# Optimization experiments

Hardware: AMD Instinct MI355X
Metric: run time of the kernel (lower is better)

The kernel has to match this reference:

```python
import jax, jax.numpy as jnp
import numpy as np

NUM_SAMPLES = 100


def setup_inputs() -> dict:
    key = jax.random.key(0)
    # [B, 2C, H, W]: first C channels are logits, last C are log-std
    inp = jax.random.normal(key, (8, 38, 256, 256), dtype=jnp.float32)
    return {"input": inp}


def reference(input):
    logits, log_std = jnp.split(input, 2, axis=-3)  # each [B, C, H, W]
    std = jnp.exp(log_std)
    keys = jax.random.split(jax.random.key(1), NUM_SAMPLES)

    def body(acc, k):
        eps = jax.random.normal(k, std.shape, dtype=std.dtype)
        acc = acc + jax.nn.softmax(logits + eps * std, axis=-3)
        return acc, None

    softmax_sum, _ = jax.lax.scan(body, jnp.zeros_like(logits), keys)
    return softmax_sum / NUM_SAMPLES
```

## Files before the change

### kernel.cpp

```cpp
#include <hip/hip_runtime.h>
#include <stdint.h>


#define NCH    19
#define HW     65536
#define NSAMP  100

__device__ __forceinline__ uint32_t rotl32(uint32_t x, uint32_t r) {
  return (x << r) | (x >> (32u - r));
}

__device__ __forceinline__ void tf2x32(uint32_t k0, uint32_t k1,
                                       uint32_t x0, uint32_t x1,
                                       uint32_t& o0, uint32_t& o1) {
  const uint32_t k2 = k0 ^ k1 ^ 0x1BD11BDAu;
#define TFRND(r) { x0 += x1; x1 = rotl32(x1, r); x1 ^= x0; }
  x0 += k0; x1 += k1;
  TFRND(13u) TFRND(15u) TFRND(26u) TFRND(6u)
  x0 += k1; x1 += k2 + 1u;
  TFRND(17u) TFRND(29u) TFRND(16u) TFRND(24u)
  x0 += k2; x1 += k0 + 2u;
  TFRND(13u) TFRND(15u) TFRND(26u) TFRND(6u)
  x0 += k0; x1 += k1 + 3u;
  TFRND(17u) TFRND(29u) TFRND(16u) TFRND(24u)
  x0 += k1; x1 += k2 + 4u;
  TFRND(13u) TFRND(15u) TFRND(26u) TFRND(6u)
  x0 += k2; x1 += k0 + 5u;
#undef TFRND
  o0 = x0; o1 = x1;
}

__device__ __forceinline__ float bits_to_eps(uint32_t bits) {
  const float lo = -0.99999994f;
  float f = __uint_as_float((bits >> 9) | 0x3F800000u) - 1.0f;
  float u = fmaf(f, 2.0f, lo);
  u = fmaxf(u, lo);
  float w = -__logf(fmaf(-u, u, 1.0f));
  float p;
  if (w < 5.0f) {
    w -= 2.5f;
    p = 2.81022636e-08f;
    p = fmaf(p, w, 3.43273939e-07f);
    p = fmaf(p, w, -3.5233877e-06f);
    p = fmaf(p, w, -4.39150654e-06f);
    p = fmaf(p, w, 0.00021858087f);
    p = fmaf(p, w, -0.00125372503f);
    p = fmaf(p, w, -0.00417768164f);
    p = fmaf(p, w, 0.246640727f);
    p = fmaf(p, w, 1.50140941f);
  } else {
    w = __fsqrt_rn(w) - 3.0f;
    p = -0.000200214257f;
    p = fmaf(p, w, 0.000100950558f);
    p = fmaf(p, w, 0.00134934322f);
    p = fmaf(p, w, -0.00367342844f);
    p = fmaf(p, w, 0.00573950773f);
    p = fmaf(p, w, -0.0076224613f);
    p = fmaf(p, w, 0.00943887047f);
    p = fmaf(p, w, 1.00167406f);
    p = fmaf(p, w, 2.83297682f);
  }
  return 1.41421356237f * (p * u);
}

__global__ __launch_bounds__(256, 2)
void HeteroscedasticSoftmax_kernel(const float* __restrict__ in,
                                   float* __restrict__ out) {
  __shared__ uint32_t sk0[NSAMP];
  __shared__ uint32_t sk1[NSAMP];
  const int t = threadIdx.x;
  if (t < NSAMP) {
    uint32_t a, b;
    tf2x32(0u, 1u, 0u, (uint32_t)t, a, b);
    sk0[t] = a;
    sk1[t] = b;
  }
  __syncthreads();

  const int gid = blockIdx.x * 256 + t;
  const int b_  = gid >> 16;
  const int hw  = gid & 65535;

  const float* pin = in + (size_t)b_ * (2 * NCH * HW) + hw;
  float lg[NCH], sd[NCH], acc[NCH];
#pragma unroll
  for (int c = 0; c < NCH; ++c) {
    lg[c]  = pin[c * HW];
    sd[c]  = __expf(pin[(NCH + c) * HW]);
    acc[c] = 0.0f;
  }

  const uint32_t jbase = (uint32_t)(b_ * NCH) * (uint32_t)HW + (uint32_t)hw;

#pragma unroll 1
  for (int s = 0; s < NSAMP; ++s) {
    const uint32_t k0 = sk0[s], k1 = sk1[s];
    float z[NCH];
    float m = -1e30f;
#pragma unroll
    for (int c = 0; c < NCH; ++c) {
      uint32_t o0, o1;
      tf2x32(k0, k1, 0u, jbase + (uint32_t)c * HW, o0, o1);
      const float eps = bits_to_eps(o0 ^ o1);
      z[c] = fmaf(eps, sd[c], lg[c]);
      m = fmaxf(m, z[c]);
    }
    float ssum = 0.0f;
#pragma unroll
    for (int c = 0; c < NCH; ++c) {
      z[c] = __expf(z[c] - m);
      ssum += z[c];
    }
    const float r = 1.0f / ssum;
#pragma unroll
    for (int c = 0; c < NCH; ++c) acc[c] = fmaf(z[c], r, acc[c]);
  }

  float* pout = out + (size_t)b_ * (NCH * HW) + hw;
#pragma unroll
  for (int c = 0; c < NCH; ++c) pout[c * HW] = acc[c] * 0.01f;
}

extern "C" void kernel_launch(void* const* d_in, const int* in_sizes, int n_in,
                              void* d_out, int out_size, void* d_ws, size_t ws_size,
                              hipStream_t stream) {
  const float* in = (const float*)d_in[0];
  float* out = (float*)d_out;
  HeteroscedasticSoftmax_kernel<<<2048, 256, 0, stream>>>(in, out);
}
```

Measured before the change: 2.328 ms.

## Fold constants and use hardware intrinsics in Threefry, erfinv and softmax

Specializes the per-element Threefry hash for a zero first counter word, folding key additions and returning the XOR of the outputs directly. Rotations become alignbit instructions. The sqrt(2) and log2(e) factors are pre-folded into the erfinv coefficients and the per-pixel logits and std, so exp2 can be used directly. Keys are loaded as wave-uniform scalars via readfirstlane, the max and sum reductions become trees, and the divide is replaced by a hardware reciprocal. The aim is fewer VALU instructions in this compute-bound loop, at the cost of small rounding differences from rescaled constants and the approximate reciprocal.

```diff
diff --git a/kernel.cpp b/kernel.cpp
--- a/kernel.cpp
+++ b/kernel.cpp
@@ -6,28 +6,60 @@
 #define HW     65536
 #define NSAMP  100
 
-__device__ __forceinline__ uint32_t rotl32(uint32_t x, uint32_t r) {
-  return (x << r) | (x >> (32u - r));
+__device__ __forceinline__ uint32_t rotl(uint32_t x, uint32_t r) {
+  return __builtin_amdgcn_alignbit(x, x, 32u - r);
 }
 
-__device__ __forceinline__ void tf2x32(uint32_t k0, uint32_t k1,
-                                       uint32_t x0, uint32_t x1,
-                                       uint32_t& o0, uint32_t& o1) {
+__device__ __forceinline__ void tf2x32_full(uint32_t k0, uint32_t k1,
+                                            uint32_t x0, uint32_t x1,
+                                            uint32_t& o0, uint32_t& o1) {
   const uint32_t k2 = k0 ^ k1 ^ 0x1BD11BDAu;
-#define TFRND(r) { x0 += x1; x1 = rotl32(x1, r); x1 ^= x0; }
+#define TFR(r) { x0 += x1; x1 = rotl(x1, r) ^ x0; }
   x0 += k0; x1 += k1;
-  TFRND(13u) TFRND(15u) TFRND(26u) TFRND(6u)
+  TFR(13u) TFR(15u) TFR(26u) TFR(6u)
   x0 += k1; x1 += k2 + 1u;
-  TFRND(17u) TFRND(29u) TFRND(16u) TFRND(24u)
+  TFR(17u) TFR(29u) TFR(16u) TFR(24u)
   x0 += k2; x1 += k0 + 2u;
-  TFRND(13u) TFRND(15u) TFRND(26u) TFRND(6u)
+  TFR(13u) TFR(15u) TFR(26u) TFR(6u)
   x0 += k0; x1 += k1 + 3u;
-  TFRND(17u) TFRND(29u) TFRND(16u) TFRND(24u)
+  TFR(17u) TFR(29u) TFR(16u) TFR(24u)
   x0 += k1; x1 += k2 + 4u;
-  TFRND(13u) TFRND(15u) TFRND(26u) TFRND(6u)
+  TFR(13u) TFR(15u) TFR(26u) TFR(6u)
   x0 += k2; x1 += k0 + 5u;
-#undef TFRND
+#undef TFR
   o0 = x0; o1 = x1;
+}
+
+__device__ __forceinline__ uint32_t tf_fold(uint32_t k0, uint32_t k1, uint32_t k2,
+                                            uint32_t x1in) {
+  uint32_t x0, x1;
+  x1 = x1in + k1;
+  x0 = k0 + x1;
+  x1 = rotl(x1, 13u) ^ x0;
+  x0 += x1; x1 = rotl(x1, 15u) ^ x0;
+  x0 += x1; x1 = rotl(x1, 26u) ^ x0;
+  x0 += x1; x1 = rotl(x1,  6u) ^ x0;
+  x1 += k2 + 1u;
+  x0 = x0 + k1 + x1; x1 = rotl(x1, 17u) ^ x0;
+  x0 += x1; x1 = rotl(x1, 29u) ^ x0;
+  x0 += x1; x1 = rotl(x1, 16u) ^ x0;
+  x0 += x1; x1 = rotl(x1, 24u) ^ x0;
+  x1 += k0 + 2u;
+  x0 = x0 + k2 + x1; x1 = rotl(x1, 13u) ^ x0;
+  x0 += x1; x1 = rotl(x1, 15u) ^ x0;
+  x0 += x1; x1 = rotl(x1, 26u) ^ x0;
+  x0 += x1; x1 = rotl(x1,  6u) ^ x0;
+  x1 += k1 + 3u;
+  x0 = x0 + k0 + x1; x1 = rotl(x1, 17u) ^ x0;
+  x0 += x1; x1 = rotl(x1, 29u) ^ x0;
+  x0 += x1; x1 = rotl(x1, 16u) ^ x0;
+  x0 += x1; x1 = rotl(x1, 24u) ^ x0;
+  x1 += k2 + 4u;
+  x0 = x0 + k1 + x1; x1 = rotl(x1, 13u) ^ x0;
+  x0 += x1; x1 = rotl(x1, 15u) ^ x0;
+  x0 += x1; x1 = rotl(x1, 26u) ^ x0;
+  x0 += x1; x1 = rotl(x1,  6u) ^ x0;
+  return (x0 + k2) ^ (x1 + k0 + 5u);
 }
 
 __device__ __forceinline__ float bits_to_eps(uint32_t bits) {
@@ -39,28 +71,28 @@
   float p;
   if (w < 5.0f) {
     w -= 2.5f;
-    p = 2.81022636e-08f;
-    p = fmaf(p, w, 3.43273939e-07f);
-    p = fmaf(p, w, -3.5233877e-06f);
-    p = fmaf(p, w, -4.39150654e-06f);
-    p = fmaf(p, w, 0.00021858087f);
-    p = fmaf(p, w, -0.00125372503f);
-    p = fmaf(p, w, -0.00417768164f);
-    p = fmaf(p, w, 0.246640727f);
-    p = fmaf(p, w, 1.50140941f);
+    p = 3.9742683e-08f;
+    p = fmaf(p, w, 4.8546493e-07f);
+    p = fmaf(p, w, -4.9828230e-06f);
+    p = fmaf(p, w, -6.2105302e-06f);
+    p = fmaf(p, w, 3.0912002e-04f);
+    p = fmaf(p, w, -1.7730354e-03f);
+    p = fmaf(p, w, -5.9081371e-03f);
+    p = fmaf(p, w, 3.4880267e-01f);
+    p = fmaf(p, w, 2.1233141e+00f);
   } else {
     w = __fsqrt_rn(w) - 3.0f;
-    p = -0.000200214257f;
-    p = fmaf(p, w, 0.000100950558f);
-    p = fmaf(p, w, 0.00134934322f);
-    p = fmaf(p, w, -0.00367342844f);
-    p = fmaf(p, w, 0.00573950773f);
-    p = fmaf(p, w, -0.0076224613f);
-    p = fmaf(p, w, 0.00943887047f);
-    p = fmaf(p, w, 1.00167406f);
-    p = fmaf(p, w, 2.83297682f);
+    p = -2.8314594e-04f;
+    p = fmaf(p, w, 1.4276565e-04f);
+    p = fmaf(p, w, 1.9082604e-03f);
+    p = fmaf(p, w, -5.1950124e-03f);
+    p = fmaf(p, w, 8.1168916e-03f);
+    p = fmaf(p, w, -1.0779791e-02f);
+    p = fmaf(p, w, 1.3348577e-02f);
+    p = fmaf(p, w, 1.4165810e+00f);
+    p = fmaf(p, w, 4.0064324e+00f);
   }
-  return 1.41421356237f * (p * u);
+  return p * u;
 }
 
 __global__ __launch_bounds__(256, 2)
@@ -71,7 +103,7 @@
   const int t = threadIdx.x;
   if (t < NSAMP) {
     uint32_t a, b;
-    tf2x32(0u, 1u, 0u, (uint32_t)t, a, b);
+    tf2x32_full(0u, 1u, 0u, (uint32_t)t, a, b);
     sk0[t] = a;
     sk1[t] = b;
   }
@@ -81,12 +113,13 @@
   const int b_  = gid >> 16;
   const int hw  = gid & 65535;
 
+  const float L2E = 1.4426950408889634f;
   const float* pin = in + (size_t)b_ * (2 * NCH * HW) + hw;
-  float lg[NCH], sd[NCH], acc[NCH];
+  float lgl[NCH], sdl[NCH], acc[NCH];
 #pragma unroll
   for (int c = 0; c < NCH; ++c) {
-    lg[c]  = pin[c * HW];
-    sd[c]  = __expf(pin[(NCH + c) * HW]);
+    lgl[c] = pin[c * HW] * L2E;
+    sdl[c] = __expf(pin[(NCH + c) * HW]) * L2E;
     acc[c] = 0.0f;
   }
 
@@ -94,24 +127,42 @@
 
 #pragma unroll 1
   for (int s = 0; s < NSAMP; ++s) {
-    const uint32_t k0 = sk0[s], k1 = sk1[s];
+    const uint32_t k0 = __builtin_amdgcn_readfirstlane(sk0[s]);
+    const uint32_t k1 = __builtin_amdgcn_readfirstlane(sk1[s]);
+    const uint32_t k2 = k0 ^ k1 ^ 0x1BD11BDAu;
+
     float z[NCH];
-    float m = -1e30f;
 #pragma unroll
     for (int c = 0; c < NCH; ++c) {
-      uint32_t o0, o1;
-      tf2x32(k0, k1, 0u, jbase + (uint32_t)c * HW, o0, o1);
-      const float eps = bits_to_eps(o0 ^ o1);
-      z[c] = fmaf(eps, sd[c], lg[c]);
-      m = fmaxf(m, z[c]);
+      const uint32_t bits = tf_fold(k0, k1, k2, jbase + (uint32_t)c * HW);
+      const float eps = bits_to_eps(bits);
+      z[c] = fmaf(eps, sdl[c], lgl[c]);
     }
-    float ssum = 0.0f;
+
+    float m0 = fmaxf(z[0], z[1]),  m1 = fmaxf(z[2], z[3]);
+    float m2 = fmaxf(z[4], z[5]),  m3 = fmaxf(z[6], z[7]);
+    float m4 = fmaxf(z[8], z[9]),  m5 = fmaxf(z[10], z[11]);
+    float m6 = fmaxf(z[12], z[13]), m7 = fmaxf(z[14], z[15]);
+    float m8 = fmaxf(z[16], z[17]);
+    m0 = fmaxf(m0, m1); m2 = fmaxf(m2, m3); m4 = fmaxf(m4, m5);
+    m6 = fmaxf(m6, m7); m8 = fmaxf(m8, z[18]);
+    m0 = fmaxf(m0, m2); m4 = fmaxf(m4, m6);
+    m0 = fmaxf(m0, m4);
+    const float m = fmaxf(m0, m8);
+
 #pragma unroll
-    for (int c = 0; c < NCH; ++c) {
-      z[c] = __expf(z[c] - m);
-      ssum += z[c];
-    }
-    const float r = 1.0f / ssum;
+    for (int c = 0; c < NCH; ++c) z[c] = __builtin_amdgcn_exp2f(z[c] - m);
+
+    float s0 = z[0] + z[1],  s1 = z[2] + z[3];
+    float s2 = z[4] + z[5],  s3 = z[6] + z[7];
+    float s4 = z[8] + z[9],  s5 = z[10] + z[11];
+    float s6 = z[12] + z[13], s7 = z[14] + z[15];
+    float s8 = z[16] + z[17];
+    s0 += s1; s2 += s3; s4 += s5; s6 += s7; s8 += z[18];
+    s0 += s2; s4 += s6;
+    s0 += s4;
+    const float r = __builtin_amdgcn_rcpf(s0 + s8);
+
 #pragma unroll
     for (int c = 0; c < NCH; ++c) acc[c] = fmaf(z[c], r, acc[c]);
   }
```

New measurement: 2.272 ms. 2.4% less time.
